# Performance work log

Measured on AMD Instinct MI355X. Metric: run time of the kernel, lower is better.

The kernel has to match this reference:

```python
import jax, jax.numpy as jnp
import numpy as np
from jax import lax

B, S, T = 32, 128, 128
V_SRC, V_TGT, E, U = 32000, 32000, 128, 256


def _lstm(xs, h0, c0, Wx, Wh, b):
    # xs: [T, B, F]; Keras gate order i, f, g(candidate), o
    def step(carry, x):
        h, c = carry
        z = x @ Wx + h @ Wh + b
        i, f, g, o = jnp.split(z, 4, axis=-1)
        c = jax.nn.sigmoid(f) * c + jax.nn.sigmoid(i) * jnp.tanh(g)
        h = jax.nn.sigmoid(o) * jnp.tanh(c)
        return (h, c), h
    (h, c), hs = lax.scan(step, (h0, c0), xs)
    return hs, h, c


def setup_inputs() -> dict:
    key = jax.random.key(0)
    ks = jax.random.split(key, 20)
    p = lambda k, shp: (jax.random.normal(k, shp, dtype=jnp.float32) * 0.02)
    return {
        "src": jax.random.randint(ks[0], (B, S), 0, V_SRC),
        "tgt": jax.random.randint(ks[1], (B, T), 0, V_TGT),
        "enc_emb": p(ks[2], (V_SRC, E)),
        "enc_Wx": p(ks[3], (E, 4 * U)),
        "enc_Wh": p(ks[4], (U, 4 * U)),
        "enc_b": jnp.zeros((4 * U,), jnp.float32),
        "dec_emb": p(ks[5], (V_TGT, E)),
        "dec_Wx": p(ks[6], (U + E, 4 * U)),
        "dec_Wh": p(ks[7], (U, 4 * U)),
        "dec_b": jnp.zeros((4 * U,), jnp.float32),
        "att_W1": p(ks[8], (U, U)),
        "att_b1": jnp.zeros((U,), jnp.float32),
        "att_W2": p(ks[9], (U, U)),
        "att_b2": jnp.zeros((U,), jnp.float32),
        "att_V": p(ks[10], (U, 1)),
        "att_bV": jnp.zeros((1,), jnp.float32),
        "fc_W": p(ks[11], (U, V_TGT)),
        "fc_b": jnp.zeros((V_TGT,), jnp.float32),
    }


def reference(src, tgt, enc_emb, enc_Wx, enc_Wh, enc_b, dec_emb, dec_Wx, dec_Wh,
              dec_b, att_W1, att_b1, att_W2, att_b2, att_V, att_bV, fc_W, fc_b):
    # ---- encoder ----
    enc_x = enc_emb[src]                                  # [B,S,E]
    enc_hs, h, c = _lstm(enc_x.transpose(1, 0, 2),
                         jnp.zeros((B, U), enc_Wx.dtype),
                         jnp.zeros((B, U), enc_Wx.dtype),
                         enc_Wx, enc_Wh, enc_b)
    enc_out = enc_hs.transpose(1, 0, 2)                   # [B,S,U]
    keys = enc_out @ att_W2 + att_b2                      # [B,S,U] (hoisted, same math)

    # ---- decoder (faithful: step 0 uses tgt[:,0]; step t>=1 uses tgt[:,t-1]) ----
    dec_tokens = jnp.concatenate([tgt[:, :1], tgt[:, :-1]], axis=1)  # [B,T]
    dec_x = dec_emb[dec_tokens].transpose(1, 0, 2)        # [T,B,E]

    def step(carry, x_emb):
        h, c = carry
        q = (h @ att_W1 + att_b1)[:, None, :]             # [B,1,U]
        score = jnp.tanh(q + keys) @ att_V + att_bV       # [B,S,1]
        attn = jax.nn.softmax(score, axis=1)
        ctx = jnp.sum(attn * enc_out, axis=1)             # [B,U]
        xin = jnp.concatenate([ctx, x_emb], axis=-1)      # [B,U+E]
        z = xin @ dec_Wx + h @ dec_Wh + dec_b
        i, f, g, o = jnp.split(z, 4, axis=-1)
        c = jax.nn.sigmoid(f) * c + jax.nn.sigmoid(i) * jnp.tanh(g)
        h = jax.nn.sigmoid(o) * jnp.tanh(c)
        probs = jax.nn.softmax(h @ fc_W + fc_b, axis=-1)  # [B,V]
        return (h, c), probs

    _, out = lax.scan(step, (h, c), dec_x)                # [T,B,V]
    return out.transpose(1, 0, 2)                         # [B,T,V]
```

## Files before the change

kernel.cpp:

```cpp
#include <hip/hip_runtime.h>
#include <hip/hip_bf16.h>
#include <hip/hip_fp16.h>
#include <cstdint>
#include <cstddef>

#define B_ 32
#define S_ 128
#define T_ 128
#define E_ 128
#define U_ 256
#define V_ 32000
#define G4 1024
#define TV 4096000

typedef __attribute__((ext_vector_type(8))) short short8_t;
typedef __attribute__((ext_vector_type(4))) float f32x4;
typedef unsigned long long u64;

static __device__ __forceinline__ unsigned short f2bf(float x) {
  union { float f; unsigned int u; } v; v.f = x;
  unsigned int r = (v.u + 0x7fffu + ((v.u >> 16) & 1u)) >> 16;
  return (unsigned short)r;
}
static __device__ __forceinline__ float sigmoidf_(float x) {
  return 1.0f / (1.0f + __expf(-x));
}
static __device__ __forceinline__ float tanhf_(float x) {
  float e = __expf(2.0f * x);
  return 1.0f - 2.0f / (e + 1.0f);
}

static __device__ __forceinline__ unsigned int f2e5(float x) {
  __half h = __float2half(x);
  __half_raw hr = *(__half_raw*)&h;
  unsigned int u = hr.x;
  unsigned int r = (u + 0x7Fu + ((u >> 8) & 1u)) >> 8;
  return r & 0xFFu;
}

static __device__ __forceinline__ unsigned pk2(float a, float b) {
  auto h = __builtin_amdgcn_cvt_pkrtz(a, b);
  return __builtin_bit_cast(unsigned, h);
}
#define SEL01 0x05000400u
#define SEL23 0x07000600u
static __device__ __forceinline__ unsigned e5pair(unsigned w, unsigned sel) {
  return __builtin_amdgcn_perm(w, 0u, sel);
}
static __device__ __forceinline__ float dot2(unsigned a, unsigned b, float c) {
  float d;
  asm("v_dot2_f32_f16 %0, %1, %2, %3" : "=v"(d) : "v"(a), "v"(b), "v"(c));
  return d;
}
static __device__ __forceinline__ unsigned pkadd(unsigned a, unsigned b) {
  unsigned d; asm("v_pk_add_f16 %0, %1, %2" : "=v"(d) : "v"(a), "v"(b)); return d;
}
static __device__ __forceinline__ unsigned pkmul(unsigned a, unsigned b) {
  unsigned d; asm("v_pk_mul_f16 %0, %1, %2" : "=v"(d) : "v"(a), "v"(b)); return d;
}
static __device__ __forceinline__ unsigned pkfma(unsigned a, unsigned b, unsigned c) {
  unsigned d; asm("v_pk_fma_f16 %0, %1, %2, %3" : "=v"(d) : "v"(a), "v"(b), "v"(c)); return d;
}
static __device__ __forceinline__ unsigned pkmax(unsigned a, unsigned b) {
  unsigned d; asm("v_pk_max_f16 %0, %1, %2" : "=v"(d) : "v"(a), "v"(b)); return d;
}
static __device__ __forceinline__ unsigned pkmin(unsigned a, unsigned b) {
  unsigned d; asm("v_pk_min_f16 %0, %1, %2" : "=v"(d) : "v"(a), "v"(b)); return d;
}

static __device__ __forceinline__ void pub64u(u64* p, unsigned val, unsigned tag) {
  u64 v = ((u64)tag << 32) | (u64)val;
  __hip_atomic_store(p, v, __ATOMIC_RELAXED, __HIP_MEMORY_SCOPE_AGENT);
}
static __device__ __forceinline__ u64 ld64(const u64* p) {
  return __hip_atomic_load(p, __ATOMIC_RELAXED, __HIP_MEMORY_SCOPE_AGENT);
}

__global__ __launch_bounds__(256) void k_prep_x(
    const int* __restrict__ src, const int* __restrict__ tgt,
    const float* __restrict__ enc_emb, const float* __restrict__ enc_Wx,
    const float* __restrict__ enc_b,
    const float* __restrict__ dec_emb, const float* __restrict__ dec_Wx,
    const float* __restrict__ dec_b,
    float* __restrict__ Xe, float* __restrict__ Xd)
{
  __shared__ float emb_l[8][E_];
  int wg = blockIdx.x;
  int tid = threadIdx.x;
  bool is_dec = (wg >= 512);
  int r0 = (is_dec ? (wg - 512) : wg) * 8;
  const float* emb  = is_dec ? dec_emb : enc_emb;
  const float* W    = is_dec ? (dec_Wx + (size_t)U_ * G4) : enc_Wx;
  const float* bias = is_dec ? dec_b : enc_b;
  float* Xout = is_dec ? Xd : Xe;

  for (int i = 0; i < 4; ++i) {
    int lin = i * 256 + tid;
    int rr = lin >> 7, k = lin & 127;
    int r = r0 + rr;
    int b = r & 31, st = r >> 5;
    int tok;
    if (is_dec) tok = tgt[b * T_ + (st > 0 ? st - 1 : 0)];
    else        tok = src[b * S_ + st];
    emb_l[rr][k] = emb[(size_t)tok * E_ + k];
  }
  __syncthreads();

  float acc[8][4];
  #pragma unroll
  for (int rr = 0; rr < 8; ++rr)
    #pragma unroll
    for (int cc = 0; cc < 4; ++cc) acc[rr][cc] = 0.f;

  for (int k = 0; k < E_; ++k) {
    float w0 = W[(size_t)k * G4 + tid];
    float w1 = W[(size_t)k * G4 + tid + 256];
    float w2 = W[(size_t)k * G4 + tid + 512];
    float w3 = W[(size_t)k * G4 + tid + 768];
    #pragma unroll
    for (int rr = 0; rr < 8; ++rr) {
      float e = emb_l[rr][k];
      acc[rr][0] += e * w0; acc[rr][1] += e * w1;
      acc[rr][2] += e * w2; acc[rr][3] += e * w3;
    }
  }
  #pragma unroll
  for (int rr = 0; rr < 8; ++rr) {
    int r = r0 + rr;
    #pragma unroll
    for (int cc = 0; cc < 4; ++cc) {
      int col = tid + cc * 256;
      Xout[(size_t)r * G4 + col] = acc[rr][cc] + bias[col];
    }
  }
}

__global__ __launch_bounds__(256) void k_prep_fcw(
    const float* __restrict__ fcW, unsigned short* __restrict__ fcWt)
{
  __shared__ float tile[64][65];
  int bid = blockIdx.x, tid = threadIdx.x;
  int n0 = (bid % 500) * 64, k0 = (bid / 500) * 64;
  for (int i = 0; i < 16; ++i) {
    int lin = i * 256 + tid;
    int k = lin >> 6, n = lin & 63;
    tile[k][n] = fcW[(size_t)(k0 + k) * V_ + n0 + n];
  }
  __syncthreads();
  for (int i = 0; i < 16; ++i) {
    int lin = i * 256 + tid;
    int n = lin >> 6, k = lin & 63;
    fcWt[(size_t)(n0 + n) * 256 + k0 + k] = f2bf(tile[k][n]);
  }
}

__global__ __launch_bounds__(1024) void k_encoder4(
    const float* __restrict__ Xe, const float* __restrict__ Wh,
    float* __restrict__ enc_out, float* __restrict__ h_state,
    float* __restrict__ c_state, u64* __restrict__ hpubE )
{
  __shared__ unsigned int WhU[64 * 256];
  __shared__ unsigned int h2[128];
  __shared__ float scr_z[4 * 256];

  int bid = blockIdx.x, tid = threadIdx.x;
  int b = bid & 31, g = bid >> 5;

  for (int idx = tid; idx < 64 * 256; idx += 1024) {
    int k4 = idx >> 8, c = idx & 255;
    int gc = (c >> 6) * 256 + g * 64 + (c & 63);
    unsigned w = 0;
    #pragma unroll
    for (int i = 0; i < 4; ++i)
      w |= f2e5(Wh[(size_t)(4 * k4 + i) * G4 + gc]) << (8 * i);
    WhU[k4 * 256 + c] = w;
  }
  float c_reg = 0.f, h_reg = 0.f;
  __syncthreads();

  for (int s = 0; s < S_; ++s) {
    if (tid < 128) {
      if (s == 0) h2[tid] = 0u;
      else {
        const u64* p = &hpubE[((size_t)(s & 1) * 32 + b) * 128 + tid];
        u64 v = ld64(p);
        while ((unsigned)(v >> 32) < (unsigned)s) { __builtin_amdgcn_s_sleep(1); v = ld64(p); }
        h2[tid] = (unsigned)v;
      }
    }
    __syncthreads();
    {
      int c = tid & 255, kq = tid >> 8;
      const unsigned* wp = &WhU[(kq * 16) * 256 + c];
      const unsigned* hh = &h2[kq * 32];
      float z0 = 0.f, z1 = 0.f;
      #pragma unroll
      for (int j = 0; j < 16; ++j) {
        unsigned w = wp[j * 256];
        z0 = dot2(e5pair(w, SEL01), hh[2 * j], z0);
        z1 = dot2(e5pair(w, SEL23), hh[2 * j + 1], z1);
      }
      scr_z[kq * 256 + c] = z0 + z1;
    }
    __syncthreads();
    if (tid < 64) {
      int r = tid, gc = g * 64 + r;
      const float* xe = Xe + (size_t)(s * B_ + b) * G4;
      float z[4];
      #pragma unroll
      for (int q = 0; q < 4; ++q) {
        int c = q * 64 + r;
        z[q] = scr_z[c] + scr_z[256 + c] + scr_z[512 + c] + scr_z[768 + c]
             + xe[q * 256 + gc];
      }
      float c = sigmoidf_(z[1]) * c_reg + sigmoidf_(z[0]) * tanhf_(z[2]);
      c_reg = c;
      float h = sigmoidf_(z[3]) * tanhf_(c);
      h_reg = h;
      enc_out[((size_t)(b * S_ + s)) * U_ + gc] = h;
      if (s < S_ - 1) {
        float hx = __shfl_xor(h, 1);
        if (!(r & 1))
          pub64u(&hpubE[((size_t)((s + 1) & 1) * 32 + b) * 128 + g * 32 + (r >> 1)],
                 pk2(h, hx), (unsigned)(s + 1));
      }
    }
    __syncthreads();
  }
  if (tid < 64) {
    h_state[b * U_ + g * 64 + tid] = h_reg;
    c_state[b * U_ + g * 64 + tid] = c_reg;
  }
}

__global__ __launch_bounds__(256) void k_keys(
    const float* __restrict__ enc_out, const float* __restrict__ W2,
    const float* __restrict__ b2,
    unsigned char* __restrict__ keys8, unsigned char* __restrict__ eo8T)
{
  __shared__ float x_l[8][U_];
  int wg = blockIdx.x, tid = threadIdx.x;
  int r0 = wg * 8;
  for (int i = 0; i < 8; ++i) x_l[i][tid] = enc_out[(size_t)(r0 + i) * U_ + tid];
  __syncthreads();
  float acc[8];
  #pragma unroll
  for (int rr = 0; rr < 8; ++rr) acc[rr] = 0.f;
  for (int k = 0; k < U_; ++k) {
    float w = W2[(size_t)k * U_ + tid];
    #pragma unroll
    for (int rr = 0; rr < 8; ++rr) acc[rr] += x_l[rr][k] * w;
  }
  float bb = b2[tid];
  #pragma unroll
  for (int rr = 0; rr < 8; ++rr) {
    int r = r0 + rr;
    keys8[(size_t)r * U_ + tid] = (unsigned char)f2e5(acc[rr] + bb);
    int bI = r >> 7, sI = r & 127;
    eo8T[((size_t)bI * U_ + tid) * S_ + sI] = (unsigned char)f2e5(x_l[rr][tid]);
  }
}

__global__ __launch_bounds__(512) void k_decoder(
    const float* __restrict__ Xd, const float* __restrict__ dec_Wx,
    const float* __restrict__ Wh,
    const float* __restrict__ W1, const float* __restrict__ b1,
    const float* __restrict__ attV, const float* __restrict__ attbV,
    const unsigned char* __restrict__ keys8, const unsigned char* __restrict__ eo8T,
    const float* __restrict__ h0, const float* __restrict__ c0,
    unsigned short* __restrict__ Hbf,
    u64* __restrict__ hpub2 )
{
  __shared__ unsigned int WxU[64 * 128];
  __shared__ unsigned int WhU[64 * 128];
  __shared__ unsigned int W1U[64 * 256];
  __shared__ float scr_zh[2 * 128];
  __shared__ float scr_c[2 * 256];
  __shared__ float scr_z[4 * 128];
  __shared__ unsigned int q2[160];
  __shared__ unsigned int aV2[160];
  __shared__ unsigned int h2[128];
  __shared__ unsigned int ctx2[128];
  __shared__ unsigned int esc2[64];
  __shared__ float escw[8];
  __shared__ float b1_l[256];

  int bid = blockIdx.x, tid = threadIdx.x;
  int b = bid & 31, g = bid >> 5;
  int lane = tid & 63, wid = tid >> 6;

  for (int idx = tid; idx < 64 * 128; idx += 512) {
    int k4 = idx >> 7, c = idx & 127;
    int gc = (c >> 5) * 256 + g * 32 + (c & 31);
    unsigned wx = 0, wh = 0;
    #pragma unroll
    for (int i = 0; i < 4; ++i) {
      int k = 4 * k4 + i;
      wx |= f2e5(dec_Wx[(size_t)k * G4 + gc]) << (8 * i);
      wh |= f2e5(Wh[(size_t)k * G4 + gc]) << (8 * i);
    }
    WxU[k4 * 128 + c] = wx;
    WhU[k4 * 128 + c] = wh;
  }
  for (int idx = tid; idx < 64 * 256; idx += 512) {
    int k4 = idx >> 8, u = idx & 255;
    unsigned w = 0;
    #pragma unroll
    for (int i = 0; i < 4; ++i)
      w |= f2e5(W1[(size_t)(4 * k4 + i) * U_ + u]) << (8 * i);
    W1U[k4 * 256 + u] = w;
  }
  if (tid < 128)
    aV2[(tid >> 5) * 40 + (tid & 31)] = pk2(attV[2 * tid], attV[2 * tid + 1]);
  if (tid < 256) b1_l[tid] = b1[tid];
  float bV = attbV[0];
  float c_reg = 0.f, h_reg = 0.f;
  if (tid < 32) {
    h_reg = h0[b * U_ + g * 32 + tid];
    c_reg = c0[b * U_ + g * 32 + tid];
  }
  __syncthreads();

  if (tid < 32) {
    float hx = __shfl_xor(h_reg, 1);
    if (!(tid & 1))
      pub64u(&hpub2[((size_t)0 * 32 + b) * 128 + g * 16 + (tid >> 1)], pk2(h_reg, hx), 1u);
  }

  const unsigned NEG1 = pk2(-1.f, -1.f), POS1 = pk2(1.f, 1.f);
  const unsigned C1 = pk2(-0.333333333f, -0.333333333f);
  const unsigned C2 = pk2(0.133333333f, 0.133333333f);
  const unsigned C3 = pk2(-0.053968254f, -0.053968254f);

  const unsigned char* kb = keys8 + (size_t)b * S_ * U_;
  const unsigned char* eb = eo8T + (size_t)b * U_ * S_;

  for (int t = 0; t < T_; ++t) {
    unsigned tag = (unsigned)(t + 1);
    int par = t & 1;

    float xd0 = 0.f, xd1 = 0.f, xd2 = 0.f, xd3 = 0.f;
    if (tid < 32) {
      const float* xd = Xd + (size_t)(t * B_ + b) * G4 + g * 32 + tid;
      xd0 = xd[0]; xd1 = xd[256]; xd2 = xd[512]; xd3 = xd[768];
    }

    if (tid < 128) {
      const u64* hp = &hpub2[((size_t)par * 32 + b) * 128 + tid];
      u64 vh = ld64(hp);
      while ((unsigned)(vh >> 32) < tag) { __builtin_amdgcn_s_sleep(1); vh = ld64(hp); }
      h2[tid] = (unsigned)vh;
    }
    __syncthreads();

    int sI = tid >> 2, uq = tid & 3;
    int uI = tid & 255, sh = tid >> 8;
    uint4 kA, kB, kC, kD, eA, eB, eC, eD;
    {
      const uint4* kp = (const uint4*)(kb + (size_t)sI * U_ + uq * 64);
      kA = kp[0]; kB = kp[1]; kC = kp[2]; kD = kp[3];
      const uint4* ep = (const uint4*)(eb + (size_t)uI * S_ + sh * 64);
      eA = ep[0]; eB = ep[1]; eC = ep[2]; eD = ep[3];
    }
    if (tid < 256) {
      int c = tid;
      float qa = 0.f, qb = 0.f;
      #pragma unroll
      for (int j = 0; j < 64; ++j) {
        unsigned w = W1U[j * 256 + c];
        qa = dot2(e5pair(w, SEL01), h2[2 * j], qa);
        qb = dot2(e5pair(w, SEL23), h2[2 * j + 1], qb);
      }
      float q = qa + qb + b1_l[c];
      float qx = __shfl_xor(q, 1);
      if (!(c & 1)) q2[(c >> 6) * 40 + ((c & 63) >> 1)] = pk2(q, qx);
    } else {
      int t2 = tid & 255;
      int c = t2 & 127, kh2 = t2 >> 7;
      const unsigned* wp = &WhU[(kh2 * 32) * 128 + c];
      const unsigned* hh = &h2[kh2 * 64];
      float z0 = 0.f, z1 = 0.f;
      #pragma unroll
      for (int j = 0; j < 32; ++j) {
        unsigned w = wp[j * 128];
        z0 = dot2(e5pair(w, SEL01), hh[2 * j], z0);
        z1 = dot2(e5pair(w, SEL23), hh[2 * j + 1], z1);
      }
      scr_zh[kh2 * 128 + c] = z0 + z1;
    }
    __syncthreads();

    {
      unsigned kw[16] = {kA.x, kA.y, kA.z, kA.w, kB.x, kB.y, kB.z, kB.w,
                         kC.x, kC.y, kC.z, kC.w, kD.x, kD.y, kD.z, kD.w};
      const unsigned* qq = &q2[uq * 40];
      const unsigned* vv = &aV2[uq * 40];
      float a0 = 0.f, a1 = 0.f;
      #pragma unroll
      for (int j = 0; j < 16; ++j) {
        unsigned w = kw[j];
        unsigned x0 = pkadd(e5pair(w, SEL01), qq[2 * j]);
        unsigned x1 = pkadd(e5pair(w, SEL23), qq[2 * j + 1]);
        x0 = pkmin(pkmax(x0, NEG1), POS1);
        x1 = pkmin(pkmax(x1, NEG1), POS1);
        unsigned s0_ = pkmul(x0, x0), s1_ = pkmul(x1, x1);
        unsigned t0 = pkfma(s0_, C3, C2), t1 = pkfma(s1_, C3, C2);
        t0 = pkfma(s0_, t0, C1); t1 = pkfma(s1_, t1, C1);
        unsigned th0 = pkfma(pkmul(x0, s0_), t0, x0);
        unsigned th1 = pkfma(pkmul(x1, s1_), t1, x1);
        a0 = dot2(th0, vv[2 * j], a0);
        a1 = dot2(th1, vv[2 * j + 1], a1);
      }
      float a = a0 + a1;
      a += __shfl_xor(a, 1); a += __shfl_xor(a, 2);
      float ea = __expf(a + bV);
      float ep = __shfl_xor(ea, 4);
      if (uq == 0 && !(sI & 1)) esc2[sI >> 1] = pk2(ea, ep);
      float dsum = ea;
      dsum += __shfl_xor(dsum, 4); dsum += __shfl_xor(dsum, 8);
      dsum += __shfl_xor(dsum, 16); dsum += __shfl_xor(dsum, 32);
      if (lane == 0) escw[wid] = dsum;
    }
    __syncthreads();

    {
      unsigned ewv[16] = {eA.x, eA.y, eA.z, eA.w, eB.x, eB.y, eB.z, eB.w,
                          eC.x, eC.y, eC.z, eC.w, eD.x, eD.y, eD.z, eD.w};
      const unsigned* e2 = &esc2[sh * 32];
      float c0a = 0.f, c1a = 0.f;
      #pragma unroll
      for (int j = 0; j < 16; ++j) {
        unsigned w = ewv[j];
        c0a = dot2(e5pair(w, SEL01), e2[2 * j], c0a);
        c1a = dot2(e5pair(w, SEL23), e2[2 * j + 1], c1a);
      }
      scr_c[sh * 256 + uI] = c0a + c1a;
    }
    __syncthreads();

    if (tid < 128) {
      int u0 = 2 * tid;
      ctx2[tid] = pk2(scr_c[u0] + scr_c[256 + u0],
                      scr_c[u0 + 1] + scr_c[256 + u0 + 1]);
    }
    __syncthreads();

    {
      float d = ((escw[0] + escw[1]) + (escw[2] + escw[3])) +
                ((escw[4] + escw[5]) + (escw[6] + escw[7]));
      float dinv = 1.0f / d;
      int c = tid & 127, kq = tid >> 7;
      const unsigned* wp = &WxU[(kq * 16) * 128 + c];
      const unsigned* cc = &ctx2[kq * 32];
      float z0 = 0.f, z1 = 0.f;
      #pragma unroll
      for (int j = 0; j < 16; ++j) {
        unsigned w = wp[j * 128];
        z0 = dot2(e5pair(w, SEL01), cc[2 * j], z0);
        z1 = dot2(e5pair(w, SEL23), cc[2 * j + 1], z1);
      }
      float zh = (kq < 2) ? scr_zh[kq * 128 + c] : 0.f;
      scr_z[kq * 128 + c] = zh + (z0 + z1) * dinv;
    }
    __syncthreads();

    if (tid < 32) {
      int r = tid, gc = g * 32 + r;
      float zi = scr_z[r]      + scr_z[128 + r]      + scr_z[256 + r]      + scr_z[384 + r]      + xd0;
      float zf = scr_z[32 + r] + scr_z[128 + 32 + r] + scr_z[256 + 32 + r] + scr_z[384 + 32 + r] + xd1;
      float zg = scr_z[64 + r] + scr_z[128 + 64 + r] + scr_z[256 + 64 + r] + scr_z[384 + 64 + r] + xd2;
      float zo = scr_z[96 + r] + scr_z[128 + 96 + r] + scr_z[256 + 96 + r] + scr_z[384 + 96 + r] + xd3;
      float c = sigmoidf_(zf) * c_reg + sigmoidf_(zi) * tanhf_(zg);
      c_reg = c;
      float h = sigmoidf_(zo) * tanhf_(c);
      h_reg = h;
      Hbf[(size_t)(t * B_ + b) * U_ + gc] = f2bf(h);
      if (t < T_ - 1) {
        int par1 = (t + 1) & 1;
        float hx = __shfl_xor(h, 1);
        if (!(r & 1))
          pub64u(&hpub2[((size_t)par1 * 32 + b) * 128 + g * 16 + (r >> 1)],
                 pk2(h, hx), (unsigned)(t + 2));
      }
    }
    __syncthreads();
  }
}

__global__ __launch_bounds__(256) void k_fc(
    const unsigned short* __restrict__ Hbf, const unsigned short* __restrict__ fcWt,
    const float* __restrict__ fcb, float* __restrict__ out,
    float* __restrict__ rs_part)
{
  __shared__ uint4 Al[128 * 8];
  __shared__ uint4 Bl[128 * 8];
  __shared__ float rsum_l[128][2];

  int bid = blockIdx.x, tid = threadIdx.x;
  int nt = bid >> 5, mt = bid & 31;
  int m0 = mt * 128, n0 = nt * 128;
  int lane = tid & 63, wave = tid >> 6;
  int wm = (wave >> 1) * 64, wn = (wave & 1) * 64;
  int g = lane >> 4, r15 = lane & 15;

  f32x4 acc[4][4];
  f32x4 zero = {0.f, 0.f, 0.f, 0.f};
  #pragma unroll
  for (int mi = 0; mi < 4; ++mi)
    #pragma unroll
    for (int ni = 0; ni < 4; ++ni) acc[mi][ni] = zero;

  const unsigned short* Ag = Hbf  + (size_t)m0 * 256;
  const unsigned short* Bg = fcWt + (size_t)n0 * 256;

  for (int kt = 0; kt < 4; ++kt) {
    int kk = kt * 64;
    #pragma unroll
    for (int blk = 0; blk < 4; ++blk) {
      int lin = blk * 256 + tid;
      int row = lin >> 3, kq = lin & 7;
      Al[row * 8 + (kq ^ (row & 7))] = *(const uint4*)(Ag + (size_t)row * 256 + kk + kq * 8);
      Bl[row * 8 + (kq ^ (row & 7))] = *(const uint4*)(Bg + (size_t)row * 256 + kk + kq * 8);
    }
    __syncthreads();
    #pragma unroll
    for (int kk2 = 0; kk2 < 2; ++kk2) {
      short8_t a[4], bfr[4];
      #pragma unroll
      for (int mi = 0; mi < 4; ++mi) {
        int row = wm + mi * 16 + r15;
        a[mi] = *(const short8_t*)&Al[row * 8 + ((kk2 * 4 + g) ^ (row & 7))];
      }
      #pragma unroll
      for (int ni = 0; ni < 4; ++ni) {
        int row = wn + ni * 16 + r15;
        bfr[ni] = *(const short8_t*)&Bl[row * 8 + ((kk2 * 4 + g) ^ (row & 7))];
      }
      #pragma unroll
      for (int mi = 0; mi < 4; ++mi)
        #pragma unroll
        for (int ni = 0; ni < 4; ++ni)
          acc[mi][ni] = __builtin_amdgcn_mfma_f32_16x16x32_bf16(a[mi], bfr[ni], acc[mi][ni], 0, 0, 0);
    }
    __syncthreads();
  }

  float fcb_l[4];
  #pragma unroll
  for (int ni = 0; ni < 4; ++ni) fcb_l[ni] = fcb[n0 + wn + ni * 16 + r15];

  #pragma unroll
  for (int mi = 0; mi < 4; ++mi) {
    #pragma unroll
    for (int jj = 0; jj < 4; ++jj) {
      int rloc = wm + mi * 16 + g * 4 + jj;
      int grow = m0 + rloc;
      int bb = grow & 31, tt = grow >> 5;
      size_t obase = (size_t)bb * TV + (size_t)tt * V_;
      float s = 0.f;
      #pragma unroll
      for (int ni = 0; ni < 4; ++ni) {
        float v = __expf(acc[mi][ni][jj] + fcb_l[ni]);
        out[obase + n0 + wn + ni * 16 + r15] = v;
        s += v;
      }
      s += __shfl_xor(s, 1); s += __shfl_xor(s, 2);
      s += __shfl_xor(s, 4); s += __shfl_xor(s, 8);
      if (r15 == 0) rsum_l[rloc][wave & 1] = s;
    }
  }
  __syncthreads();
  if (tid < 128)
    rs_part[(size_t)nt * 4096 + m0 + tid] = rsum_l[tid][0] + rsum_l[tid][1];
}

__global__ __launch_bounds__(256) void k_rowsum(
    const float* __restrict__ rs_part, float* __restrict__ row_inv)
{
  int gidx = blockIdx.x * 256 + threadIdx.x;
  float s = 0.f;
  for (int nt = 0; nt < 250; ++nt) s += rs_part[(size_t)nt * 4096 + gidx];
  row_inv[gidx] = 1.0f / s;
}

__global__ __launch_bounds__(256) void k_norm(
    float4* __restrict__ out4, const float* __restrict__ row_inv)
{
  const long total = 32768000;
  long stride = (long)gridDim.x * 256;
  for (long i = (long)blockIdx.x * 256 + threadIdx.x; i < total; i += stride) {
    long flat = i * 4;
    int bb = (int)(flat / TV);
    int rem = (int)(flat % TV);
    int tt = rem / V_;
    float sc = row_inv[tt * 32 + bb];
    float4 v = out4[i];
    v.x *= sc; v.y *= sc; v.z *= sc; v.w *= sc;
    out4[i] = v;
  }
}

extern "C" void kernel_launch(void* const* d_in, const int* in_sizes, int n_in,
                              void* d_out, int out_size, void* d_ws, size_t ws_size,
                              hipStream_t stream) {
  (void)in_sizes; (void)n_in; (void)out_size; (void)ws_size;
  const int*   src     = (const int*)d_in[0];
  const int*   tgt     = (const int*)d_in[1];
  const float* enc_emb = (const float*)d_in[2];
  const float* enc_Wx  = (const float*)d_in[3];
  const float* enc_Wh  = (const float*)d_in[4];
  const float* enc_b   = (const float*)d_in[5];
  const float* dec_emb = (const float*)d_in[6];
  const float* dec_Wx  = (const float*)d_in[7];
  const float* dec_Wh  = (const float*)d_in[8];
  const float* dec_b   = (const float*)d_in[9];
  const float* att_W1  = (const float*)d_in[10];
  const float* att_b1  = (const float*)d_in[11];
  const float* att_W2  = (const float*)d_in[12];
  const float* att_b2  = (const float*)d_in[13];
  const float* att_V   = (const float*)d_in[14];
  const float* att_bV  = (const float*)d_in[15];
  const float* fc_W    = (const float*)d_in[16];
  const float* fc_b    = (const float*)d_in[17];
  float* out = (float*)d_out;

  char* ws = (char*)d_ws;
  size_t o = 0;
  auto alloc = [&](size_t bytes) {
    char* p = ws + o;
    o = (o + bytes + 255) & ~(size_t)255;
    return p;
  };
  float*          Xe      = (float*)alloc((size_t)S_ * B_ * G4 * 4);
  float*          Xd      = (float*)alloc((size_t)T_ * B_ * G4 * 4);
  float*          enc_out = (float*)alloc((size_t)B_ * S_ * U_ * 4);
  unsigned char*  keys8   = (unsigned char*)alloc((size_t)B_ * S_ * U_);
  unsigned char*  eo8T    = (unsigned char*)alloc((size_t)B_ * U_ * S_);
  unsigned short* Hbf     = (unsigned short*)alloc((size_t)T_ * B_ * U_ * 2);
  unsigned short* fcWt    = (unsigned short*)alloc((size_t)V_ * U_ * 2);
  float*          h_state = (float*)alloc((size_t)B_ * U_ * 4);
  float*          c_state = (float*)alloc((size_t)B_ * U_ * 4);
  float*          rs_part = (float*)alloc((size_t)250 * 4096 * 4);
  float*          row_inv = (float*)alloc((size_t)4096 * 4);
  size_t pub_off = o;
  u64* hpubE = (u64*)alloc((size_t)2 * 32 * 128 * 8);
  u64* hpub2 = (u64*)alloc((size_t)2 * 32 * 128 * 8);
  size_t pub_bytes = o - pub_off;

  hipMemsetAsync(ws + pub_off, 0, pub_bytes, stream);
  hipLaunchKernelGGL(k_prep_x, dim3(1024), dim3(256), 0, stream,
                     src, tgt, enc_emb, enc_Wx, enc_b, dec_emb, dec_Wx, dec_b, Xe, Xd);
  hipLaunchKernelGGL(k_prep_fcw, dim3(2000), dim3(256), 0, stream, fc_W, fcWt);
  hipLaunchKernelGGL(k_encoder4, dim3(128), dim3(1024), 0, stream,
                     Xe, enc_Wh, enc_out, h_state, c_state, hpubE);
  hipLaunchKernelGGL(k_keys, dim3(512), dim3(256), 0, stream,
                     enc_out, att_W2, att_b2, keys8, eo8T);
  hipLaunchKernelGGL(k_decoder, dim3(256), dim3(512), 0, stream,
                     Xd, dec_Wx, dec_Wh, att_W1, att_b1, att_V, att_bV,
                     keys8, eo8T, h_state, c_state, Hbf, hpub2);
  hipLaunchKernelGGL(k_fc, dim3(8000), dim3(256), 0, stream,
                     Hbf, fcWt, fc_b, out, rs_part);
  hipLaunchKernelGGL(k_rowsum, dim3(16), dim3(256), 0, stream, rs_part, row_inv);
  hipLaunchKernelGGL(k_norm, dim3(2048), dim3(256), 0, stream,
                     (float4*)d_out, row_inv);
}
```

Measured before the change: 1.502 ms.

## Split encoder across 256 blocks and widen decoder to 1024 threads

The encoder recurrence now runs on 256 blocks, each owning 32 hidden units instead of 64, and each thread handles a shorter 8-deep K slice. The step's x-projection load is prefetched before the h wait. The decoder block doubles to 1024 threads: the query projection splits K over four groups with a reduction pass, attention scoring and context use 8 and 4 way splits, and the Wh and Wx gate matvecs are fused into one 8-way split loop. This shortens the per-step serial latency of both recurrences. In exchange it adds cross-block synchronisation traffic, an extra barrier for the q reduction, and more partial-sum reduction work.

```diff
diff --git a/kernel.cpp b/kernel.cpp
--- a/kernel.cpp
+++ b/kernel.cpp
@@ -154,31 +154,36 @@
   }
 }
 
-__global__ __launch_bounds__(1024) void k_encoder4(
+__global__ __launch_bounds__(1024) void k_encoder8(
     const float* __restrict__ Xe, const float* __restrict__ Wh,
     float* __restrict__ enc_out, float* __restrict__ h_state,
     float* __restrict__ c_state, u64* __restrict__ hpubE )
 {
-  __shared__ unsigned int WhU[64 * 256];
+  __shared__ unsigned int WhU[64 * 128];
   __shared__ unsigned int h2[128];
-  __shared__ float scr_z[4 * 256];
+  __shared__ float scr_z[8 * 128];
 
   int bid = blockIdx.x, tid = threadIdx.x;
   int b = bid & 31, g = bid >> 5;
 
-  for (int idx = tid; idx < 64 * 256; idx += 1024) {
-    int k4 = idx >> 8, c = idx & 255;
-    int gc = (c >> 6) * 256 + g * 64 + (c & 63);
+  for (int idx = tid; idx < 64 * 128; idx += 1024) {
+    int k4 = idx >> 7, c = idx & 127;
+    int gc = (c >> 5) * 256 + g * 32 + (c & 31);
     unsigned w = 0;
     #pragma unroll
     for (int i = 0; i < 4; ++i)
       w |= f2e5(Wh[(size_t)(4 * k4 + i) * G4 + gc]) << (8 * i);
-    WhU[k4 * 256 + c] = w;
+    WhU[k4 * 128 + c] = w;
   }
   float c_reg = 0.f, h_reg = 0.f;
   __syncthreads();
 
   for (int s = 0; s < S_; ++s) {
+    float xe0 = 0.f, xe1 = 0.f, xe2 = 0.f, xe3 = 0.f;
+    if (tid < 32) {
+      const float* xe = Xe + (size_t)(s * B_ + b) * G4 + g * 32 + tid;
+      xe0 = xe[0]; xe1 = xe[256]; xe2 = xe[512]; xe3 = xe[768];
+    }
     if (tid < 128) {
       if (s == 0) h2[tid] = 0u;
       else {
@@ -190,28 +195,27 @@
     }
     __syncthreads();
     {
-      int c = tid & 255, kq = tid >> 8;
-      const unsigned* wp = &WhU[(kq * 16) * 256 + c];
-      const unsigned* hh = &h2[kq * 32];
+      int c = tid & 127, k8 = tid >> 7;
+      const unsigned* wp = &WhU[(k8 * 8) * 128 + c];
+      const unsigned* hh = &h2[k8 * 16];
       float z0 = 0.f, z1 = 0.f;
       #pragma unroll
-      for (int j = 0; j < 16; ++j) {
-        unsigned w = wp[j * 256];
+      for (int j = 0; j < 8; ++j) {
+        unsigned w = wp[j * 128];
         z0 = dot2(e5pair(w, SEL01), hh[2 * j], z0);
         z1 = dot2(e5pair(w, SEL23), hh[2 * j + 1], z1);
       }
-      scr_z[kq * 256 + c] = z0 + z1;
-    }
-    __syncthreads();
-    if (tid < 64) {
-      int r = tid, gc = g * 64 + r;
-      const float* xe = Xe + (size_t)(s * B_ + b) * G4;
-      float z[4];
+      scr_z[k8 * 128 + c] = z0 + z1;
+    }
+    __syncthreads();
+    if (tid < 32) {
+      int r = tid, gc = g * 32 + r;
+      float z[4] = {xe0, xe1, xe2, xe3};
       #pragma unroll
       for (int q = 0; q < 4; ++q) {
-        int c = q * 64 + r;
-        z[q] = scr_z[c] + scr_z[256 + c] + scr_z[512 + c] + scr_z[768 + c]
-             + xe[q * 256 + gc];
+        int c = q * 32 + r;
+        #pragma unroll
+        for (int k8 = 0; k8 < 8; ++k8) z[q] += scr_z[k8 * 128 + c];
       }
       float c = sigmoidf_(z[1]) * c_reg + sigmoidf_(z[0]) * tanhf_(z[2]);
       c_reg = c;
@@ -221,15 +225,15 @@
       if (s < S_ - 1) {
         float hx = __shfl_xor(h, 1);
         if (!(r & 1))
-          pub64u(&hpubE[((size_t)((s + 1) & 1) * 32 + b) * 128 + g * 32 + (r >> 1)],
+          pub64u(&hpubE[((size_t)((s + 1) & 1) * 32 + b) * 128 + g * 16 + (r >> 1)],
                  pk2(h, hx), (unsigned)(s + 1));
       }
     }
     __syncthreads();
   }
-  if (tid < 64) {
-    h_state[b * U_ + g * 64 + tid] = h_reg;
-    c_state[b * U_ + g * 64 + tid] = c_reg;
+  if (tid < 32) {
+    h_state[b * U_ + g * 32 + tid] = h_reg;
+    c_state[b * U_ + g * 32 + tid] = c_reg;
   }
 }
 
@@ -261,7 +265,7 @@
   }
 }
 
-__global__ __launch_bounds__(512) void k_decoder(
+__global__ __launch_bounds__(1024) void k_decoder(
     const float* __restrict__ Xd, const float* __restrict__ dec_Wx,
     const float* __restrict__ Wh,
     const float* __restrict__ W1, const float* __restrict__ b1,
@@ -274,22 +278,22 @@
   __shared__ unsigned int WxU[64 * 128];
   __shared__ unsigned int WhU[64 * 128];
   __shared__ unsigned int W1U[64 * 256];
-  __shared__ float scr_zh[2 * 128];
-  __shared__ float scr_c[2 * 256];
-  __shared__ float scr_z[4 * 128];
+  __shared__ float scr_q[4 * 256];
+  __shared__ float scr_c[4 * 256];
+  __shared__ float scr_z[8 * 128];
   __shared__ unsigned int q2[160];
   __shared__ unsigned int aV2[160];
   __shared__ unsigned int h2[128];
   __shared__ unsigned int ctx2[128];
   __shared__ unsigned int esc2[64];
-  __shared__ float escw[8];
+  __shared__ float escw[16];
   __shared__ float b1_l[256];
 
   int bid = blockIdx.x, tid = threadIdx.x;
   int b = bid & 31, g = bid >> 5;
   int lane = tid & 63, wid = tid >> 6;
 
-  for (int idx = tid; idx < 64 * 128; idx += 512) {
+  for (int idx = tid; idx < 64 * 128; idx += 1024) {
     int k4 = idx >> 7, c = idx & 127;
     int gc = (c >> 5) * 256 + g * 32 + (c & 31);
     unsigned wx = 0, wh = 0;
@@ -302,7 +306,7 @@
     WxU[k4 * 128 + c] = wx;
     WhU[k4 * 128 + c] = wh;
   }
-  for (int idx = tid; idx < 64 * 256; idx += 512) {
+  for (int idx = tid; idx < 64 * 256; idx += 1024) {
     int k4 = idx >> 8, u = idx & 255;
     unsigned w = 0;
     #pragma unroll
@@ -310,8 +314,10 @@
       w |= f2e5(W1[(size_t)(4 * k4 + i) * U_ + u]) << (8 * i);
     W1U[k4 * 256 + u] = w;
   }
-  if (tid < 128)
-    aV2[(tid >> 5) * 40 + (tid & 31)] = pk2(attV[2 * tid], attV[2 * tid + 1]);
+  if (tid < 128) {
+    int p = tid;
+    aV2[(p >> 4) * 20 + (p & 15)] = pk2(attV[2 * p], attV[2 * p + 1]);
+  }
   if (tid < 256) b1_l[tid] = b1[tid];
   float bV = attbV[0];
   float c_reg = 0.f, h_reg = 0.f;
@@ -353,51 +359,45 @@
     }
     __syncthreads();
 
-    int sI = tid >> 2, uq = tid & 3;
-    int uI = tid & 255, sh = tid >> 8;
-    uint4 kA, kB, kC, kD, eA, eB, eC, eD;
+    int sI = tid >> 3, uo = tid & 7;
+    int uI = tid & 255, sq = tid >> 8;
+    uint4 kA, kB, eA, eB;
     {
-      const uint4* kp = (const uint4*)(kb + (size_t)sI * U_ + uq * 64);
-      kA = kp[0]; kB = kp[1]; kC = kp[2]; kD = kp[3];
-      const uint4* ep = (const uint4*)(eb + (size_t)uI * S_ + sh * 64);
-      eA = ep[0]; eB = ep[1]; eC = ep[2]; eD = ep[3];
-    }
-    if (tid < 256) {
-      int c = tid;
+      const uint4* kp = (const uint4*)(kb + (size_t)sI * U_ + uo * 32);
+      kA = kp[0]; kB = kp[1];
+      const uint4* ep = (const uint4*)(eb + (size_t)uI * S_ + sq * 32);
+      eA = ep[0]; eB = ep[1];
+    }
+    {
+      int c = tid & 255, kq = tid >> 8;
+      const unsigned* wp = &W1U[(kq * 16) * 256 + c];
+      const unsigned* hh = &h2[kq * 32];
       float qa = 0.f, qb = 0.f;
       #pragma unroll
-      for (int j = 0; j < 64; ++j) {
-        unsigned w = W1U[j * 256 + c];
-        qa = dot2(e5pair(w, SEL01), h2[2 * j], qa);
-        qb = dot2(e5pair(w, SEL23), h2[2 * j + 1], qb);
-      }
-      float q = qa + qb + b1_l[c];
-      float qx = __shfl_xor(q, 1);
-      if (!(c & 1)) q2[(c >> 6) * 40 + ((c & 63) >> 1)] = pk2(q, qx);
-    } else {
-      int t2 = tid & 255;
-      int c = t2 & 127, kh2 = t2 >> 7;
-      const unsigned* wp = &WhU[(kh2 * 32) * 128 + c];
-      const unsigned* hh = &h2[kh2 * 64];
-      float z0 = 0.f, z1 = 0.f;
-      #pragma unroll
-      for (int j = 0; j < 32; ++j) {
-        unsigned w = wp[j * 128];
-        z0 = dot2(e5pair(w, SEL01), hh[2 * j], z0);
-        z1 = dot2(e5pair(w, SEL23), hh[2 * j + 1], z1);
-      }
-      scr_zh[kh2 * 128 + c] = z0 + z1;
+      for (int j = 0; j < 16; ++j) {
+        unsigned w = wp[j * 256];
+        qa = dot2(e5pair(w, SEL01), hh[2 * j], qa);
+        qb = dot2(e5pair(w, SEL23), hh[2 * j + 1], qb);
+      }
+      scr_q[kq * 256 + c] = qa + qb;
+    }
+    __syncthreads();
+
+    if (tid < 128) {
+      int u0 = 2 * tid;
+      float q0 = scr_q[u0] + scr_q[256 + u0] + scr_q[512 + u0] + scr_q[768 + u0] + b1_l[u0];
+      float q1 = scr_q[u0 + 1] + scr_q[256 + u0 + 1] + scr_q[512 + u0 + 1] + scr_q[768 + u0 + 1] + b1_l[u0 + 1];
+      q2[(tid >> 4) * 20 + (tid & 15)] = pk2(q0, q1);
     }
     __syncthreads();
 
     {
-      unsigned kw[16] = {kA.x, kA.y, kA.z, kA.w, kB.x, kB.y, kB.z, kB.w,
-                         kC.x, kC.y, kC.z, kC.w, kD.x, kD.y, kD.z, kD.w};
-      const unsigned* qq = &q2[uq * 40];
-      const unsigned* vv = &aV2[uq * 40];
+      unsigned kw[8] = {kA.x, kA.y, kA.z, kA.w, kB.x, kB.y, kB.z, kB.w};
+      const unsigned* qq = &q2[uo * 20];
+      const unsigned* vv = &aV2[uo * 20];
       float a0 = 0.f, a1 = 0.f;
       #pragma unroll
-      for (int j = 0; j < 16; ++j) {
+      for (int j = 0; j < 8; ++j) {
         unsigned w = kw[j];
         unsigned x0 = pkadd(e5pair(w, SEL01), qq[2 * j]);
         unsigned x1 = pkadd(e5pair(w, SEL23), qq[2 * j + 1]);
@@ -412,67 +412,74 @@
         a1 = dot2(th1, vv[2 * j + 1], a1);
       }
       float a = a0 + a1;
-      a += __shfl_xor(a, 1); a += __shfl_xor(a, 2);
+      a += __shfl_xor(a, 1); a += __shfl_xor(a, 2); a += __shfl_xor(a, 4);
       float ea = __expf(a + bV);
-      float ep = __shfl_xor(ea, 4);
-      if (uq == 0 && !(sI & 1)) esc2[sI >> 1] = pk2(ea, ep);
+      float ep = __shfl_xor(ea, 8);
+      if (uo == 0 && !(sI & 1)) esc2[sI >> 1] = pk2(ea, ep);
       float dsum = ea;
-      dsum += __shfl_xor(dsum, 4); dsum += __shfl_xor(dsum, 8);
-      dsum += __shfl_xor(dsum, 16); dsum += __shfl_xor(dsum, 32);
+      dsum += __shfl_xor(dsum, 8); dsum += __shfl_xor(dsum, 16); dsum += __shfl_xor(dsum, 32);
       if (lane == 0) escw[wid] = dsum;
     }
     __syncthreads();
 
     {
-      unsigned ewv[16] = {eA.x, eA.y, eA.z, eA.w, eB.x, eB.y, eB.z, eB.w,
-                          eC.x, eC.y, eC.z, eC.w, eD.x, eD.y, eD.z, eD.w};
-      const unsigned* e2 = &esc2[sh * 32];
+      unsigned ewv[8] = {eA.x, eA.y, eA.z, eA.w, eB.x, eB.y, eB.z, eB.w};
+      const unsigned* e2 = &esc2[sq * 16];
       float c0a = 0.f, c1a = 0.f;
       #pragma unroll
-      for (int j = 0; j < 16; ++j) {
+      for (int j = 0; j < 8; ++j) {
         unsigned w = ewv[j];
         c0a = dot2(e5pair(w, SEL01), e2[2 * j], c0a);
         c1a = dot2(e5pair(w, SEL23), e2[2 * j + 1], c1a);
       }
-      scr_c[sh * 256 + uI] = c0a + c1a;
+      scr_c[sq * 256 + uI] = c0a + c1a;
     }
     __syncthreads();
 
     if (tid < 128) {
       int u0 = 2 * tid;
-      ctx2[tid] = pk2(scr_c[u0] + scr_c[256 + u0],
-                      scr_c[u0 + 1] + scr_c[256 + u0 + 1]);
+      float ca = scr_c[u0] + scr_c[256 + u0] + scr_c[512 + u0] + scr_c[768 + u0];
+      float cb = scr_c[u0 + 1] + scr_c[256 + u0 + 1] + scr_c[512 + u0 + 1] + scr_c[768 + u0 + 1];
+      ctx2[tid] = pk2(ca, cb);
     }
     __syncthreads();
 
     {
       float d = ((escw[0] + escw[1]) + (escw[2] + escw[3])) +
-                ((escw[4] + escw[5]) + (escw[6] + escw[7]));
+                ((escw[4] + escw[5]) + (escw[6] + escw[7])) +
+                ((escw[8] + escw[9]) + (escw[10] + escw[11])) +
+                ((escw[12] + escw[13]) + (escw[14] + escw[15]));
       float dinv = 1.0f / d;
-      int c = tid & 127, kq = tid >> 7;
-      const unsigned* wp = &WxU[(kq * 16) * 128 + c];
-      const unsigned* cc = &ctx2[kq * 32];
-      float z0 = 0.f, z1 = 0.f;
-      #pragma unroll
-      for (int j = 0; j < 16; ++j) {
-        unsigned w = wp[j * 128];
-        z0 = dot2(e5pair(w, SEL01), cc[2 * j], z0);
-        z1 = dot2(e5pair(w, SEL23), cc[2 * j + 1], z1);
-      }
-      float zh = (kq < 2) ? scr_zh[kq * 128 + c] : 0.f;
-      scr_z[kq * 128 + c] = zh + (z0 + z1) * dinv;
+      int c = tid & 127, k8 = tid >> 7;
+      const unsigned* wxp = &WxU[(k8 * 8) * 128 + c];
+      const unsigned* whp = &WhU[(k8 * 8) * 128 + c];
+      const unsigned* cc = &ctx2[k8 * 16];
+      const unsigned* hh = &h2[k8 * 16];
+      float zx0 = 0.f, zx1 = 0.f, zh0 = 0.f, zh1 = 0.f;
+      #pragma unroll
+      for (int j = 0; j < 8; ++j) {
+        unsigned wx = wxp[j * 128], wh = whp[j * 128];
+        zx0 = dot2(e5pair(wx, SEL01), cc[2 * j], zx0);
+        zx1 = dot2(e5pair(wx, SEL23), cc[2 * j + 1], zx1);
+        zh0 = dot2(e5pair(wh, SEL01), hh[2 * j], zh0);
+        zh1 = dot2(e5pair(wh, SEL23), hh[2 * j + 1], zh1);
+      }
+      scr_z[k8 * 128 + c] = (zh0 + zh1) + (zx0 + zx1) * dinv;
     }
     __syncthreads();
 
     if (tid < 32) {
       int r = tid, gc = g * 32 + r;
-      float zi = scr_z[r]      + scr_z[128 + r]      + scr_z[256 + r]      + scr_z[384 + r]      + xd0;
-      float zf = scr_z[32 + r] + scr_z[128 + 32 + r] + scr_z[256 + 32 + r] + scr_z[384 + 32 + r] + xd1;
-      float zg = scr_z[64 + r] + scr_z[128 + 64 + r] + scr_z[256 + 64 + r] + scr_z[384 + 64 + r] + xd2;
-      float zo = scr_z[96 + r] + scr_z[128 + 96 + r] + scr_z[256 + 96 + r] + scr_z[384 + 96 + r] + xd3;
-      float c = sigmoidf_(zf) * c_reg + sigmoidf_(zi) * tanhf_(zg);
+      float z[4] = {xd0, xd1, xd2, xd3};
+      #pragma unroll
+      for (int q = 0; q < 4; ++q) {
+        int c = q * 32 + r;
+        #pragma unroll
+        for (int k8 = 0; k8 < 8; ++k8) z[q] += scr_z[k8 * 128 + c];
+      }
+      float c = sigmoidf_(z[1]) * c_reg + sigmoidf_(z[0]) * tanhf_(z[2]);
       c_reg = c;
-      float h = sigmoidf_(zo) * tanhf_(c);
+      float h = sigmoidf_(z[3]) * tanhf_(c);
       h_reg = h;
       Hbf[(size_t)(t * B_ + b) * U_ + gc] = f2bf(h);
       if (t < T_ - 1) {
@@ -651,11 +658,11 @@
   hipLaunchKernelGGL(k_prep_x, dim3(1024), dim3(256), 0, stream,
                      src, tgt, enc_emb, enc_Wx, enc_b, dec_emb, dec_Wx, dec_b, Xe, Xd);
   hipLaunchKernelGGL(k_prep_fcw, dim3(2000), dim3(256), 0, stream, fc_W, fcWt);
-  hipLaunchKernelGGL(k_encoder4, dim3(128), dim3(1024), 0, stream,
+  hipLaunchKernelGGL(k_encoder8, dim3(256), dim3(1024), 0, stream,
                      Xe, enc_Wh, enc_out, h_state, c_state, hpubE);
   hipLaunchKernelGGL(k_keys, dim3(512), dim3(256), 0, stream,
                      enc_out, att_W2, att_b2, keys8, eo8T);
-  hipLaunchKernelGGL(k_decoder, dim3(256), dim3(512), 0, stream,
+  hipLaunchKernelGGL(k_decoder, dim3(256), dim3(1024), 0, stream,
                      Xd, dec_Wx, dec_Wh, att_W1, att_b1, att_V, att_bV,
                      keys8, eo8T, h_state, c_state, Hbf, hpub2);
   hipLaunchKernelGGL(k_fc, dim3(8000), dim3(256), 0, stream,
```

New measurement: 1.430 ms. 1.05x faster.
